# Kernel tuning notes

Measured on AMD Instinct MI355X. Metric: run time of the kernel, lower is better.

## Reference

```python
import jax, jax.numpy as jnp
import numpy as np

P, N, M = 4, 8192, 8192

def setup_inputs() -> dict:
    key = jax.random.key(0)
    k1, k2, k3, k4, k5 = jax.random.split(key, 5)
    return {
        "camera_pts": jax.random.normal(k1, (P, N, 3), dtype=jnp.float32),
        "cad_pts": jax.random.normal(k2, (P, M, 3), dtype=jnp.float32),
        "part_weight": jax.random.uniform(k3, (P,), dtype=jnp.float32),
        "rot_quat": jax.random.normal(k4, (P, 4), dtype=jnp.float32),
        "tra": jax.random.normal(k5, (P, 3, 1), dtype=jnp.float32),
    }

def _quat_to_rot(q):
    # q: [P,4] in (w,x,y,z) order, normalized outside
    a, b, c, d = q[:, 0], q[:, 1], q[:, 2], q[:, 3]
    rows = jnp.stack([
        1 - 2*c*c - 2*d*d, 2*b*c - 2*a*d,     2*a*c + 2*b*d,
        2*b*c + 2*a*d,     1 - 2*b*b - 2*d*d, 2*c*d - 2*a*b,
        2*b*d - 2*a*c,     2*a*b + 2*c*d,     1 - 2*b*b - 2*c*c,
    ], axis=-1)  # [P,9]
    return rows.reshape(-1, 3, 3)

def _chamfer(x, y):
    # x: [N,4], y: [M,4] -> scalar bidirectional chamfer (Euclidean, not squared)
    x2 = jnp.sum(x * x, axis=-1)              # [N]
    y2 = jnp.sum(y * y, axis=-1)              # [M]
    d2 = x2[:, None] + y2[None, :] - 2.0 * (x @ y.T)
    dist = jnp.sqrt(jnp.clip(d2, 0.0))        # [N,M]
    return jnp.mean(jnp.min(dist, axis=1)) + jnp.mean(jnp.min(dist, axis=0))

def reference(camera_pts, cad_pts, part_weight, rot_quat, tra):
    q = rot_quat / jnp.linalg.norm(rot_quat, axis=1, keepdims=True)
    rot = _quat_to_rot(q)                                       # [P,3,3]
    top = jnp.concatenate([rot, tra], axis=2)                   # [P,3,4]
    bottom = jnp.broadcast_to(jnp.array([[[0.0, 0.0, 0.0, 1.0]]], dtype=rot.dtype), (rot.shape[0], 1, 4))
    transforms = jnp.concatenate([top, bottom], axis=1)         # [P,4,4]
    ones_cad = jnp.ones(cad_pts.shape[:-1] + (1,), dtype=cad_pts.dtype)
    ones_cam = jnp.ones(camera_pts.shape[:-1] + (1,), dtype=camera_pts.dtype)
    cad_h = jnp.concatenate([cad_pts, ones_cad], axis=-1)       # [P,M,4]
    cam_h = jnp.concatenate([camera_pts, ones_cam], axis=-1)    # [P,N,4]
    cad_base = jnp.einsum('pij,pmj->pmi', transforms, cad_h)    # [P,M,4]
    cd = jax.vmap(_chamfer)(cad_base, cam_h)                    # [P]
    all_objective = jnp.sum(part_weight * cd)
    return all_objective, jax.lax.stop_gradient(transforms)
```

## Files before the change

### kernel.cpp

```cpp
#include <hip/hip_runtime.h>
#include <math.h>

#define NP 4
#define NN 8192
#define NM 8192

#define MINA_OFF ((NP * NM + NP * NN) * 4)
#define MINB_OFF (MINA_OFF + NP * NM)

#define TQ 4
#define QT 1024
#define SPLITS 16
#define CHUNK 512

#define RED_BLOCKS 128

__device__ inline void make_transform(const float* __restrict__ quat,
                                      const float* __restrict__ tra,
                                      int p, float T[12]) {
    float q0 = quat[p * 4 + 0], q1 = quat[p * 4 + 1];
    float q2 = quat[p * 4 + 2], q3 = quat[p * 4 + 3];
    float inv = 1.0f / sqrtf(q0 * q0 + q1 * q1 + q2 * q2 + q3 * q3);
    float a = q0 * inv, b = q1 * inv, c = q2 * inv, d = q3 * inv;
    T[0] = 1.0f - 2.0f * c * c - 2.0f * d * d;
    T[1] = 2.0f * b * c - 2.0f * a * d;
    T[2] = 2.0f * a * c + 2.0f * b * d;
    T[3] = tra[p * 3 + 0];
    T[4] = 2.0f * b * c + 2.0f * a * d;
    T[5] = 1.0f - 2.0f * b * b - 2.0f * d * d;
    T[6] = 2.0f * c * d - 2.0f * a * b;
    T[7] = tra[p * 3 + 1];
    T[8] = 2.0f * b * d - 2.0f * a * c;
    T[9] = 2.0f * a * b + 2.0f * c * d;
    T[10] = 1.0f - 2.0f * b * b - 2.0f * c * c;
    T[11] = tra[p * 3 + 2];
}

__global__ __launch_bounds__(256) void prep_kernel(
    const float* __restrict__ cam, const float* __restrict__ cad,
    const float* __restrict__ quat, const float* __restrict__ tra,
    float* __restrict__ ws, float* __restrict__ out) {
    int idx = blockIdx.x * 256 + threadIdx.x;
    const float INF = __uint_as_float(0x7f800000u);

    if (idx < NP * NM) {
        int p = idx >> 13;
        int m = idx & (NM - 1);
        float T[12];
        make_transform(quat, tra, p, T);
        float x = cad[(p * NM + m) * 3 + 0];
        float y = cad[(p * NM + m) * 3 + 1];
        float z = cad[(p * NM + m) * 3 + 2];
        float vx = fmaf(T[0], x, fmaf(T[1], y, fmaf(T[2], z, T[3])));
        float vy = fmaf(T[4], x, fmaf(T[5], y, fmaf(T[6], z, T[7])));
        float vz = fmaf(T[8], x, fmaf(T[9], y, fmaf(T[10], z, T[11])));
        float h = 0.5f * (vx * vx + vy * vy + vz * vz);
        ((float4*)ws)[idx] = make_float4(vx, vy, vz, h);
        ws[MINA_OFF + idx] = INF;
    } else {
        int k = idx - NP * NM;
        int p = k >> 13;
        int n = k & (NN - 1);
        float vx = cam[(p * NN + n) * 3 + 0];
        float vy = cam[(p * NN + n) * 3 + 1];
        float vz = cam[(p * NN + n) * 3 + 2];
        float h = 0.5f * (vx * vx + vy * vy + vz * vz);
        ((float4*)ws)[idx] = make_float4(vx, vy, vz, h);
        ws[MINB_OFF + k] = INF;
    }

    if (idx < 64) {
        int p2 = idx >> 4;
        int r = (idx >> 2) & 3;
        int c = idx & 3;
        float T[12];
        make_transform(quat, tra, p2, T);
        float v;
        if (r == 3)
            v = (c == 3) ? 1.0f : 0.0f;
        else
            v = T[r * 4 + c];
        out[1 + idx] = v;
    } else if (idx == 64) {
        out[0] = 0.0f;
    }
}

__global__ __launch_bounds__(256) void minpass_kernel(float* __restrict__ ws) {
    int tid = threadIdx.x;
    int p = blockIdx.z >> 1;
    int role = blockIdx.z & 1;

    const float4* Q;
    const float4* T;
    float* minarr;
    if (role == 0) {
        Q = (const float4*)ws + p * NM;
        T = (const float4*)ws + NP * NM + p * NN;
        minarr = ws + MINA_OFF + p * NM;
    } else {
        Q = (const float4*)ws + NP * NM + p * NN;
        T = (const float4*)ws + p * NM;
        minarr = ws + MINB_OFF + p * NN;
    }

    __shared__ float4 sT[CHUNK];

    int q0 = blockIdx.x * QT + tid;
    float4 q[TQ];
    float tmin[TQ];
#pragma unroll
    for (int k = 0; k < TQ; ++k) {
        q[k] = Q[q0 + k * 256];
        tmin[k] = __uint_as_float(0x7f800000u);
    }

    int tstart = blockIdx.y * CHUNK;
#pragma unroll
    for (int j = tid; j < CHUNK; j += 256) sT[j] = T[tstart + j];
    __syncthreads();

#pragma unroll 4
    for (int j = 0; j < CHUNK; ++j) {
        float4 t = sT[j];
#pragma unroll
        for (int k = 0; k < TQ; ++k) {
            float s = fmaf(-q[k].x, t.x, fmaf(-q[k].y, t.y, fmaf(-q[k].z, t.z, t.w)));
            tmin[k] = fminf(tmin[k], s);
        }
    }

#pragma unroll
    for (int k = 0; k < TQ; ++k) {
        float d2 = 2.0f * (q[k].w + tmin[k]);
        d2 = fmaxf(d2, 0.0f);
        atomicMin((unsigned int*)&minarr[q0 + k * 256], __float_as_uint(d2));
    }
}

__global__ __launch_bounds__(256) void finalize_kernel(
    const float* __restrict__ ws, const float* __restrict__ w,
    float* __restrict__ out) {
    const float* vals = ws + MINA_OFF;
    int i = blockIdx.x * 256 + threadIdx.x;
    int tid = threadIdx.x;

    float w0 = w[0], w1 = w[1], w2 = w[2], w3 = w[3];
    float wl[4] = {w0, w1, w2, w3};

    int i2 = i + 32768;
    float acc = wl[(i >> 13) & 3] * sqrtf(vals[i]) +
                wl[(i2 >> 13) & 3] * sqrtf(vals[i2]);

#pragma unroll
    for (int off = 32; off > 0; off >>= 1) acc += __shfl_down(acc, off, 64);

    __shared__ float wsum[4];
    if ((tid & 63) == 0) wsum[tid >> 6] = acc;
    __syncthreads();
    if (tid == 0) {
        float blocksum = (wsum[0] + wsum[1] + wsum[2] + wsum[3]) * (1.0f / 8192.0f);
        atomicAdd(out, blocksum);
    }
}

extern "C" void kernel_launch(void* const* d_in, const int* in_sizes, int n_in,
                              void* d_out, int out_size, void* d_ws, size_t ws_size,
                              hipStream_t stream) {
    const float* cam = (const float*)d_in[0];
    const float* cad = (const float*)d_in[1];
    const float* w = (const float*)d_in[2];
    const float* quat = (const float*)d_in[3];
    const float* tra = (const float*)d_in[4];
    float* out = (float*)d_out;
    float* ws = (float*)d_ws;

    prep_kernel<<<(NP * (NM + NN)) / 256, 256, 0, stream>>>(cam, cad, quat, tra, ws, out);

    dim3 grid(NM / QT, SPLITS, 2 * NP);
    minpass_kernel<<<grid, 256, 0, stream>>>(ws);

    finalize_kernel<<<RED_BLOCKS, 256, 0, stream>>>(ws, w, out);
}
```

Measured before the change: 109.3 us.

## Fuse point transform into chamfer kernel, raise per-thread queries, use v_min3

The prep pass that wrote transformed float4 points to the workspace is removed. Each chamfer block now reads the raw xyz points and applies the rigid transform and half-norm on the fly, for both its query registers and its shared-memory tile, so the init kernel only fills the min arrays with infinity and writes the transform output. Queries per thread go from 4 to 8 (QT 2048), which halves the block count and raises register use. The inner loop handles two targets per step and merges them with a single v_min3 instruction. The aim is to cut workspace traffic and ALU work per pair, at the cost of redundant transform math and lower occupancy.

```diff
diff --git a/kernel.cpp b/kernel.cpp
--- a/kernel.cpp
+++ b/kernel.cpp
@@ -5,15 +5,20 @@
 #define NN 8192
 #define NM 8192
 
-#define MINA_OFF ((NP * NM + NP * NN) * 4)
-#define MINB_OFF (MINA_OFF + NP * NM)
-
-#define TQ 4
-#define QT 1024
+#define MINB_OFF (NP * NM)
+
+#define TQ 8
+#define QT 2048
 #define SPLITS 16
 #define CHUNK 512
 
 #define RED_BLOCKS 128
+
+__device__ inline float min3f(float a, float b, float c) {
+    float d;
+    asm("v_min3_f32 %0, %1, %2, %3" : "=v"(d) : "v"(a), "v"(b), "v"(c));
+    return d;
+}
 
 __device__ inline void make_transform(const float* __restrict__ quat,
                                       const float* __restrict__ tra,
@@ -36,97 +41,109 @@
     T[11] = tra[p * 3 + 2];
 }
 
-__global__ __launch_bounds__(256) void prep_kernel(
-    const float* __restrict__ cam, const float* __restrict__ cad,
+__global__ __launch_bounds__(256) void init_kernel(
     const float* __restrict__ quat, const float* __restrict__ tra,
     float* __restrict__ ws, float* __restrict__ out) {
     int idx = blockIdx.x * 256 + threadIdx.x;
     const float INF = __uint_as_float(0x7f800000u);
-
-    if (idx < NP * NM) {
-        int p = idx >> 13;
-        int m = idx & (NM - 1);
-        float T[12];
-        make_transform(quat, tra, p, T);
-        float x = cad[(p * NM + m) * 3 + 0];
-        float y = cad[(p * NM + m) * 3 + 1];
-        float z = cad[(p * NM + m) * 3 + 2];
-        float vx = fmaf(T[0], x, fmaf(T[1], y, fmaf(T[2], z, T[3])));
-        float vy = fmaf(T[4], x, fmaf(T[5], y, fmaf(T[6], z, T[7])));
-        float vz = fmaf(T[8], x, fmaf(T[9], y, fmaf(T[10], z, T[11])));
-        float h = 0.5f * (vx * vx + vy * vy + vz * vz);
-        ((float4*)ws)[idx] = make_float4(vx, vy, vz, h);
-        ws[MINA_OFF + idx] = INF;
-    } else {
-        int k = idx - NP * NM;
-        int p = k >> 13;
-        int n = k & (NN - 1);
-        float vx = cam[(p * NN + n) * 3 + 0];
-        float vy = cam[(p * NN + n) * 3 + 1];
-        float vz = cam[(p * NN + n) * 3 + 2];
-        float h = 0.5f * (vx * vx + vy * vy + vz * vz);
-        ((float4*)ws)[idx] = make_float4(vx, vy, vz, h);
-        ws[MINB_OFF + k] = INF;
-    }
-
-    if (idx < 64) {
-        int p2 = idx >> 4;
-        int r = (idx >> 2) & 3;
-        int c = idx & 3;
-        float T[12];
-        make_transform(quat, tra, p2, T);
-        float v;
-        if (r == 3)
-            v = (c == 3) ? 1.0f : 0.0f;
-        else
-            v = T[r * 4 + c];
-        out[1 + idx] = v;
-    } else if (idx == 64) {
-        out[0] = 0.0f;
-    }
-}
-
-__global__ __launch_bounds__(256) void minpass_kernel(float* __restrict__ ws) {
+    ((float4*)ws)[idx] = make_float4(INF, INF, INF, INF);
+
+    if (blockIdx.x == 0) {
+        int t = threadIdx.x;
+        if (t < 64) {
+            int p2 = t >> 4;
+            int r = (t >> 2) & 3;
+            int c = t & 3;
+            float T[12];
+            make_transform(quat, tra, p2, T);
+            float v;
+            if (r == 3)
+                v = (c == 3) ? 1.0f : 0.0f;
+            else
+                v = T[r * 4 + c];
+            out[1 + t] = v;
+        } else if (t == 64) {
+            out[0] = 0.0f;
+        }
+    }
+}
+
+__global__ __launch_bounds__(256) void chamfer_kernel(
+    const float* __restrict__ cam, const float* __restrict__ cad,
+    const float* __restrict__ quat, const float* __restrict__ tra,
+    float* __restrict__ ws) {
     int tid = threadIdx.x;
     int p = blockIdx.z >> 1;
     int role = blockIdx.z & 1;
 
-    const float4* Q;
-    const float4* T;
+    float T[12];
+    make_transform(quat, tra, p, T);
+
+    const float* Qsrc;
+    const float* Tsrc;
     float* minarr;
     if (role == 0) {
-        Q = (const float4*)ws + p * NM;
-        T = (const float4*)ws + NP * NM + p * NN;
-        minarr = ws + MINA_OFF + p * NM;
+        Qsrc = cad + p * NM * 3;
+        Tsrc = cam + p * NN * 3;
+        minarr = ws + p * NM;
     } else {
-        Q = (const float4*)ws + NP * NM + p * NN;
-        T = (const float4*)ws + p * NM;
+        Qsrc = cam + p * NN * 3;
+        Tsrc = cad + p * NM * 3;
         minarr = ws + MINB_OFF + p * NN;
     }
 
     __shared__ float4 sT[CHUNK];
 
+    const float INF = __uint_as_float(0x7f800000u);
     int q0 = blockIdx.x * QT + tid;
     float4 q[TQ];
     float tmin[TQ];
 #pragma unroll
     for (int k = 0; k < TQ; ++k) {
-        q[k] = Q[q0 + k * 256];
-        tmin[k] = __uint_as_float(0x7f800000u);
+        int m = q0 + k * 256;
+        float x = Qsrc[m * 3 + 0];
+        float y = Qsrc[m * 3 + 1];
+        float z = Qsrc[m * 3 + 2];
+        float vx, vy, vz;
+        if (role == 0) {
+            vx = fmaf(T[0], x, fmaf(T[1], y, fmaf(T[2], z, T[3])));
+            vy = fmaf(T[4], x, fmaf(T[5], y, fmaf(T[6], z, T[7])));
+            vz = fmaf(T[8], x, fmaf(T[9], y, fmaf(T[10], z, T[11])));
+        } else {
+            vx = x; vy = y; vz = z;
+        }
+        q[k] = make_float4(vx, vy, vz, 0.5f * (vx * vx + vy * vy + vz * vz));
+        tmin[k] = INF;
     }
 
     int tstart = blockIdx.y * CHUNK;
 #pragma unroll
-    for (int j = tid; j < CHUNK; j += 256) sT[j] = T[tstart + j];
+    for (int j = tid; j < CHUNK; j += 256) {
+        int t = tstart + j;
+        float x = Tsrc[t * 3 + 0];
+        float y = Tsrc[t * 3 + 1];
+        float z = Tsrc[t * 3 + 2];
+        float vx, vy, vz;
+        if (role == 1) {
+            vx = fmaf(T[0], x, fmaf(T[1], y, fmaf(T[2], z, T[3])));
+            vy = fmaf(T[4], x, fmaf(T[5], y, fmaf(T[6], z, T[7])));
+            vz = fmaf(T[8], x, fmaf(T[9], y, fmaf(T[10], z, T[11])));
+        } else {
+            vx = x; vy = y; vz = z;
+        }
+        sT[j] = make_float4(vx, vy, vz, 0.5f * (vx * vx + vy * vy + vz * vz));
+    }
     __syncthreads();
 
 #pragma unroll 4
-    for (int j = 0; j < CHUNK; ++j) {
-        float4 t = sT[j];
+    for (int j = 0; j < CHUNK; j += 2) {
+        float4 t0 = sT[j];
+        float4 t1 = sT[j + 1];
 #pragma unroll
         for (int k = 0; k < TQ; ++k) {
-            float s = fmaf(-q[k].x, t.x, fmaf(-q[k].y, t.y, fmaf(-q[k].z, t.z, t.w)));
-            tmin[k] = fminf(tmin[k], s);
+            float s0 = fmaf(-q[k].x, t0.x, fmaf(-q[k].y, t0.y, fmaf(-q[k].z, t0.z, t0.w)));
+            float s1 = fmaf(-q[k].x, t1.x, fmaf(-q[k].y, t1.y, fmaf(-q[k].z, t1.z, t1.w)));
+            tmin[k] = min3f(tmin[k], s0, s1);
         }
     }
 
@@ -141,12 +158,11 @@
 __global__ __launch_bounds__(256) void finalize_kernel(
     const float* __restrict__ ws, const float* __restrict__ w,
     float* __restrict__ out) {
-    const float* vals = ws + MINA_OFF;
+    const float* vals = ws;
     int i = blockIdx.x * 256 + threadIdx.x;
     int tid = threadIdx.x;
 
-    float w0 = w[0], w1 = w[1], w2 = w[2], w3 = w[3];
-    float wl[4] = {w0, w1, w2, w3};
+    float wl[4] = {w[0], w[1], w[2], w[3]};
 
     int i2 = i + 32768;
     float acc = wl[(i >> 13) & 3] * sqrtf(vals[i]) +
@@ -175,10 +191,10 @@
     float* out = (float*)d_out;
     float* ws = (float*)d_ws;
 
-    prep_kernel<<<(NP * (NM + NN)) / 256, 256, 0, stream>>>(cam, cad, quat, tra, ws, out);
+    init_kernel<<<64, 256, 0, stream>>>(quat, tra, ws, out);
 
     dim3 grid(NM / QT, SPLITS, 2 * NP);
-    minpass_kernel<<<grid, 256, 0, stream>>>(ws);
+    chamfer_kernel<<<grid, 256, 0, stream>>>(cam, cad, quat, tra, ws);
 
     finalize_kernel<<<RED_BLOCKS, 256, 0, stream>>>(ws, w, out);
 }
```

Result: no change. 107.2 us (-2.0%).

## Read targets via uniform global loads and fold pairs with v_min3 in chamfer pass

Applied to the files above, without the earlier changes.

The min-distance kernel no longer stages target points in shared memory. Each thread reads target float4s straight from global memory at block-uniform addresses, which the compiler can turn into scalar loads. Each thread now holds 8 query points instead of 4, with a shorter span of targets per block and more splits, and two candidates are folded per step with the v_min3_f32 instruction. This removes the LDS traffic and the barrier and cuts min instructions, at the cost of more registers per thread and twice as many atomicMin writes.

```diff
diff --git a/kernel.cpp b/kernel.cpp
--- a/kernel.cpp
+++ b/kernel.cpp
@@ -5,15 +5,23 @@
 #define NN 8192
 #define NM 8192
 
-#define MINA_OFF ((NP * NM + NP * NN) * 4)
-#define MINB_OFF (MINA_OFF + NP * NM)
+#define PK_A_F4 0
+#define PK_B_F4 (NP * NM)
+#define MINS_OFF ((NP * NM + NP * NN) * 4)
+#define MINB_REL (NP * NM)
 
-#define TQ 4
-#define QT 1024
-#define SPLITS 16
-#define CHUNK 512
+#define TQ 8
+#define QT 2048
+#define SPLITS 32
+#define SPAN 256
 
 #define RED_BLOCKS 128
+
+__device__ inline float min3f(float a, float b, float c) {
+    float d;
+    asm("v_min3_f32 %0, %1, %2, %3" : "=v"(d) : "v"(a), "v"(b), "v"(c));
+    return d;
+}
 
 __device__ inline void make_transform(const float* __restrict__ quat,
                                       const float* __restrict__ tra,
@@ -55,18 +63,16 @@
         float vy = fmaf(T[4], x, fmaf(T[5], y, fmaf(T[6], z, T[7])));
         float vz = fmaf(T[8], x, fmaf(T[9], y, fmaf(T[10], z, T[11])));
         float h = 0.5f * (vx * vx + vy * vy + vz * vz);
-        ((float4*)ws)[idx] = make_float4(vx, vy, vz, h);
-        ws[MINA_OFF + idx] = INF;
+        ((float4*)ws)[PK_A_F4 + idx] = make_float4(vx, vy, vz, h);
+        ws[MINS_OFF + idx] = INF;
     } else {
         int k = idx - NP * NM;
-        int p = k >> 13;
-        int n = k & (NN - 1);
-        float vx = cam[(p * NN + n) * 3 + 0];
-        float vy = cam[(p * NN + n) * 3 + 1];
-        float vz = cam[(p * NN + n) * 3 + 2];
+        float vx = cam[k * 3 + 0];
+        float vy = cam[k * 3 + 1];
+        float vz = cam[k * 3 + 2];
         float h = 0.5f * (vx * vx + vy * vy + vz * vz);
-        ((float4*)ws)[idx] = make_float4(vx, vy, vz, h);
-        ws[MINB_OFF + k] = INF;
+        ((float4*)ws)[PK_B_F4 + k] = make_float4(vx, vy, vz, h);
+        ws[MINS_OFF + MINB_REL + k] = INF;
     }
 
     if (idx < 64) {
@@ -86,7 +92,8 @@
     }
 }
 
-__global__ __launch_bounds__(256) void minpass_kernel(float* __restrict__ ws) {
+__global__ __launch_bounds__(256) void chamfer_kernel(
+    const float4* __restrict__ packed, float* __restrict__ mins) {
     int tid = threadIdx.x;
     int p = blockIdx.z >> 1;
     int role = blockIdx.z & 1;
@@ -95,44 +102,41 @@
     const float4* T;
     float* minarr;
     if (role == 0) {
-        Q = (const float4*)ws + p * NM;
-        T = (const float4*)ws + NP * NM + p * NN;
-        minarr = ws + MINA_OFF + p * NM;
+        Q = packed + PK_A_F4 + p * NM;
+        T = packed + PK_B_F4 + p * NN;
+        minarr = mins + p * NM;
     } else {
-        Q = (const float4*)ws + NP * NM + p * NN;
-        T = (const float4*)ws + p * NM;
-        minarr = ws + MINB_OFF + p * NN;
+        Q = packed + PK_B_F4 + p * NN;
+        T = packed + PK_A_F4 + p * NM;
+        minarr = mins + MINB_REL + p * NN;
     }
 
-    __shared__ float4 sT[CHUNK];
-
+    const float INF = __uint_as_float(0x7f800000u);
     int q0 = blockIdx.x * QT + tid;
-    float4 q[TQ];
-    float tmin[TQ];
+    float qx[TQ], qy[TQ], qz[TQ], qw[TQ], tmin[TQ];
 #pragma unroll
     for (int k = 0; k < TQ; ++k) {
-        q[k] = Q[q0 + k * 256];
-        tmin[k] = __uint_as_float(0x7f800000u);
+        float4 v = Q[q0 + k * 256];
+        qx[k] = v.x; qy[k] = v.y; qz[k] = v.z; qw[k] = v.w;
+        tmin[k] = INF;
     }
 
-    int tstart = blockIdx.y * CHUNK;
-#pragma unroll
-    for (int j = tid; j < CHUNK; j += 256) sT[j] = T[tstart + j];
-    __syncthreads();
-
+    int tbase = blockIdx.y * SPAN;
 #pragma unroll 4
-    for (int j = 0; j < CHUNK; ++j) {
-        float4 t = sT[j];
+    for (int j = 0; j < SPAN; j += 2) {
+        float4 t0 = T[tbase + j];
+        float4 t1 = T[tbase + j + 1];
 #pragma unroll
         for (int k = 0; k < TQ; ++k) {
-            float s = fmaf(-q[k].x, t.x, fmaf(-q[k].y, t.y, fmaf(-q[k].z, t.z, t.w)));
-            tmin[k] = fminf(tmin[k], s);
+            float s0 = fmaf(-qx[k], t0.x, fmaf(-qy[k], t0.y, fmaf(-qz[k], t0.z, t0.w)));
+            float s1 = fmaf(-qx[k], t1.x, fmaf(-qy[k], t1.y, fmaf(-qz[k], t1.z, t1.w)));
+            tmin[k] = min3f(tmin[k], s0, s1);
         }
     }
 
 #pragma unroll
     for (int k = 0; k < TQ; ++k) {
-        float d2 = 2.0f * (q[k].w + tmin[k]);
+        float d2 = 2.0f * (qw[k] + tmin[k]);
         d2 = fmaxf(d2, 0.0f);
         atomicMin((unsigned int*)&minarr[q0 + k * 256], __float_as_uint(d2));
     }
@@ -141,12 +145,11 @@
 __global__ __launch_bounds__(256) void finalize_kernel(
     const float* __restrict__ ws, const float* __restrict__ w,
     float* __restrict__ out) {
-    const float* vals = ws + MINA_OFF;
+    const float* vals = ws + MINS_OFF;
     int i = blockIdx.x * 256 + threadIdx.x;
     int tid = threadIdx.x;
 
-    float w0 = w[0], w1 = w[1], w2 = w[2], w3 = w[3];
-    float wl[4] = {w0, w1, w2, w3};
+    float wl[4] = {w[0], w[1], w[2], w[3]};
 
     int i2 = i + 32768;
     float acc = wl[(i >> 13) & 3] * sqrtf(vals[i]) +
@@ -178,7 +181,7 @@
     prep_kernel<<<(NP * (NM + NN)) / 256, 256, 0, stream>>>(cam, cad, quat, tra, ws, out);
 
     dim3 grid(NM / QT, SPLITS, 2 * NP);
-    minpass_kernel<<<grid, 256, 0, stream>>>(ws);
+    chamfer_kernel<<<grid, 256, 0, stream>>>((const float4*)ws, ws + MINS_OFF);
 
     finalize_kernel<<<RED_BLOCKS, 256, 0, stream>>>(ws, w, out);
 }
```

New measurement: 127.6 us. +16.7%, slower.
